# Kernel optimization log

Hardware: AMD Instinct MI355X
Metric: run time of the kernel (lower is better)

## Reference

```python
import jax, jax.numpy as jnp
import numpy as np

KW, KH = 8, 8   # kernel_size = (kw, kh) per torch module indexing
SW, SH = 4, 4   # stride_size = (sw, sh)


def setup_inputs() -> dict:
    key = jax.random.key(0)
    x = jax.random.normal(key, (4, 128, 128, 128), dtype=jnp.float32)  # [B, C, H, W]
    return {"x": x}


def _local_autocorr(x, kh=KH, kw=KW, sh=SH, sw=SW):
    B, C, H, W = x.shape
    nh = (H - kh) // sh + 1
    nw = (W - kw) // sw + 1
    # Background is x zero-padded by (kh//2, (kh+1)//2 - 1) vertically and
    # (kw//2, (kw+1)//2 - 1) horizontally -> background patches are (2kh-1, 2kw-1).
    xp = jnp.pad(x, ((0, 0), (0, 0),
                     (kh // 2, (kh + 1) // 2 - 1),
                     (kw // 2, (kw + 1) // 2 - 1)))

    # For each shift (dy, dx) in [0,kh)x[0,kw):
    #   ret[b,iy,ix,c,dy,dx] = sum_{u,v} x[b,c,top+u,left+v] * xp[b,c,top+dy+u,left+dx+v]
    # i.e. elementwise product with the shifted map, then sum-pool with window (kh,kw), stride (sh,sw).
    def step(carry, s):
        dy = s // kw
        dx = s % kw
        shifted = jax.lax.dynamic_slice(xp, (0, 0, dy, dx), (B, C, H, W))
        prod = x * shifted
        pooled = jax.lax.reduce_window(prod, 0.0, jax.lax.add,
                                       (1, 1, kh, kw), (1, 1, sh, sw), 'VALID')
        return carry, pooled  # [B, C, nh, nw]

    _, stacked = jax.lax.scan(step, None, jnp.arange(kh * kw))
    # stacked: [kh*kw, B, C, nh, nw] with shift index s = dy*kw + dx
    out = stacked.reshape(kh, kw, B, C, nh, nw)
    out = jnp.transpose(out, (2, 4, 5, 3, 0, 1))  # [B, nh, nw, C, kh, kw]
    return out


def reference(x):
    return _local_autocorr(x)
```

## Files before the change

### kernel.cpp

```cpp
#include <hip/hip_runtime.h>


#define Cn 128
#define Hn 128
#define Wn 128
#define NH 31
#define NW 31
#define CB 4
#define PXT 8
#define PYT 4
#define TROWS 27
#define RST 44
#define CSTF4 310
#define F4C (TROWS*11)

__global__ __launch_bounds__(256)
void lac_kernel(const float* __restrict__ x, float* __restrict__ out) {
    __shared__ float sm[CB * CSTF4 * 4];

    const int bid = blockIdx.x;
    const int lg = ((bid & 7) << 9) | (bid >> 3);
    const int tx = lg & 3;
    const int ty = (lg >> 2) & 7;
    const int ct = (lg >> 5) & 31;
    const int b  = lg >> 10;
    const int c0 = ct * CB;
    const int gy0 = ty * (PYT * 4) - 4;
    const int gx0 = tx * (PXT * 4) - 4;
    const int tid = threadIdx.x;

    const bool interior = (gy0 >= 0) & (gy0 + TROWS <= Hn) & (gx0 >= 0) & (gx0 + RST <= Wn);
    if (interior) {
        for (int i = tid; i < CB * F4C; i += 256) {
            const int c   = i / F4C;
            const int rem = i - c * F4C;
            const int r   = rem / 11;
            const int q   = rem - r * 11;
            const float* src = x + (((size_t)(b * Cn + c0 + c) * Hn + gy0 + r) * Wn + gx0 + q * 4);
            reinterpret_cast<float4*>(sm)[c * CSTF4 + r * 11 + q] =
                *reinterpret_cast<const float4*>(src);
        }
    } else {
        for (int i = tid; i < CB * F4C; i += 256) {
            const int c   = i / F4C;
            const int rem = i - c * F4C;
            const int r   = rem / 11;
            const int q   = rem - r * 11;
            const int y   = gy0 + r;
            const int xc  = gx0 + q * 4;
            const float* src = x + (((size_t)(b * Cn + c0 + c) * Hn + y) * Wn + xc);
            float4 v;
            if (y >= 0 && y < Hn && xc >= 0 && xc + 3 < Wn) {
                v = *reinterpret_cast<const float4*>(src);
            } else if (y >= 0 && y < Hn) {
                v.x = (xc + 0 >= 0 && xc + 0 < Wn) ? src[0] : 0.0f;
                v.y = (xc + 1 >= 0 && xc + 1 < Wn) ? src[1] : 0.0f;
                v.z = (xc + 2 >= 0 && xc + 2 < Wn) ? src[2] : 0.0f;
                v.w = (xc + 3 >= 0 && xc + 3 < Wn) ? src[3] : 0.0f;
            } else {
                v = make_float4(0.0f, 0.0f, 0.0f, 0.0f);
            }
            reinterpret_cast<float4*>(sm)[c * CSTF4 + r * 11 + q] = v;
        }
    }
    __syncthreads();

    const int cs   = tid & 3;
    const int px   = (tid >> 2) & 7;
    const int py   = (tid >> 5) & 3;
    const int half = tid >> 7;
    const float* rg = &sm[cs * (CSTF4 * 4) + (py * 4) * RST + px * 4];

    float acc[4][8];
#pragma unroll
    for (int i = 0; i < 4; ++i)
#pragma unroll
        for (int j = 0; j < 8; ++j) acc[i][j] = 0.0f;

    float ks[4][8];

#define LOAD_RW(R)                                                              \
    float rw[16];                                                               \
    {                                                                           \
        float4 q0 = *reinterpret_cast<const float4*>(&rg[(R) * RST + 0]);       \
        float4 q1 = *reinterpret_cast<const float4*>(&rg[(R) * RST + 4]);       \
        float4 q2 = *reinterpret_cast<const float4*>(&rg[(R) * RST + 8]);       \
        float4 q3 = *reinterpret_cast<const float4*>(&rg[(R) * RST + 12]);      \
        rw[0]=q0.x; rw[1]=q0.y; rw[2]=q0.z; rw[3]=q0.w;                         \
        rw[4]=q1.x; rw[5]=q1.y; rw[6]=q1.z; rw[7]=q1.w;                         \
        rw[8]=q2.x; rw[9]=q2.y; rw[10]=q2.z; rw[11]=q2.w;                       \
        rw[12]=q3.x; rw[13]=q3.y; rw[14]=q3.z; rw[15]=q3.w;                     \
    }

    if (half == 0) {
#pragma unroll
        for (int ii = 0; ii < 12; ++ii) {
            const int R = 11 - ii;
            LOAD_RW(R)
#pragma unroll
            for (int d = 0; d < 4; ++d) {
                if (R >= d && R <= 7 + d) {
#pragma unroll
                    for (int v = 0; v < 8; ++v) {
                        const float bv = ks[(R - d) & 3][v];
#pragma unroll
                        for (int dx = 0; dx < 8; ++dx)
                            acc[d][dx] = fmaf(bv, rw[dx + v], acc[d][dx]);
                    }
                }
            }
#pragma unroll
            for (int v = 0; v < 8; ++v) ks[R & 3][v] = rw[4 + v];
        }
    } else {
#pragma unroll
        for (int ii = 0; ii < 11; ++ii) {
            const int R = 4 + ii;
            LOAD_RW(R)
#pragma unroll
            for (int d = 0; d < 4; ++d) {
                if (R >= 4 + d && R <= 11 + d) {
#pragma unroll
                    for (int v = 0; v < 8; ++v) {
                        const float bv = (d == 0) ? rw[4 + v] : ks[(R - d) & 3][v];
#pragma unroll
                        for (int dx = 0; dx < 8; ++dx)
                            acc[d][dx] = fmaf(bv, rw[dx + v], acc[d][dx]);
                    }
                }
            }
#pragma unroll
            for (int v = 0; v < 8; ++v) ks[R & 3][v] = rw[4 + v];
        }
    }
#undef LOAD_RW

    const int iy = ty * PYT + py;
    const int ix = tx * PXT + px;
    if (iy < NH && ix < NW) {
        float* o = out + ((((size_t)b * NH + iy) * NW + ix) * Cn + (c0 + cs)) * 64
                       + half * 32;
#pragma unroll
        for (int d = 0; d < 4; ++d) {
            *reinterpret_cast<float4*>(o + d * 8 + 0) =
                make_float4(acc[d][0], acc[d][1], acc[d][2], acc[d][3]);
            *reinterpret_cast<float4*>(o + d * 8 + 4) =
                make_float4(acc[d][4], acc[d][5], acc[d][6], acc[d][7]);
        }
    }
}

extern "C" void kernel_launch(void* const* d_in, const int* in_sizes, int n_in,
                              void* d_out, int out_size, void* d_ws, size_t ws_size,
                              hipStream_t stream) {
    const float* x = (const float*)d_in[0];
    float* out = (float*)d_out;
    lac_kernel<<<dim3(4096), dim3(256), 0, stream>>>(x, out);
}
```

Baseline: 89.85 us.

## Load input rows directly from global memory, dropping shared-memory staging

Removes the cooperative shared-memory tile load and barrier, so each thread reads its 16-wide input rows straight from global memory with bounds handling per row. This eliminates LDS traffic, the sync, and the shared-memory footprint, which may raise occupancy. In exchange each input element is fetched several times by different threads and relies on L1/L2 caching, with less coalesced access since the four lanes sharing a pixel read different channel planes.

```diff
diff --git a/kernel.cpp b/kernel.cpp
--- a/kernel.cpp
+++ b/kernel.cpp
@@ -9,15 +9,10 @@
 #define CB 4
 #define PXT 8
 #define PYT 4
-#define TROWS 27
-#define RST 44
-#define CSTF4 310
-#define F4C (TROWS*11)
+#define RSPAN 43
 
 __global__ __launch_bounds__(256)
 void lac_kernel(const float* __restrict__ x, float* __restrict__ out) {
-    __shared__ float sm[CB * CSTF4 * 4];
-
     const int bid = blockIdx.x;
     const int lg = ((bid & 7) << 9) | (bid >> 3);
     const int tx = lg & 3;
@@ -29,47 +24,15 @@
     const int gx0 = tx * (PXT * 4) - 4;
     const int tid = threadIdx.x;
 
-    const bool interior = (gy0 >= 0) & (gy0 + TROWS <= Hn) & (gx0 >= 0) & (gx0 + RST <= Wn);
-    if (interior) {
-        for (int i = tid; i < CB * F4C; i += 256) {
-            const int c   = i / F4C;
-            const int rem = i - c * F4C;
-            const int r   = rem / 11;
-            const int q   = rem - r * 11;
-            const float* src = x + (((size_t)(b * Cn + c0 + c) * Hn + gy0 + r) * Wn + gx0 + q * 4);
-            reinterpret_cast<float4*>(sm)[c * CSTF4 + r * 11 + q] =
-                *reinterpret_cast<const float4*>(src);
-        }
-    } else {
-        for (int i = tid; i < CB * F4C; i += 256) {
-            const int c   = i / F4C;
-            const int rem = i - c * F4C;
-            const int r   = rem / 11;
-            const int q   = rem - r * 11;
-            const int y   = gy0 + r;
-            const int xc  = gx0 + q * 4;
-            const float* src = x + (((size_t)(b * Cn + c0 + c) * Hn + y) * Wn + xc);
-            float4 v;
-            if (y >= 0 && y < Hn && xc >= 0 && xc + 3 < Wn) {
-                v = *reinterpret_cast<const float4*>(src);
-            } else if (y >= 0 && y < Hn) {
-                v.x = (xc + 0 >= 0 && xc + 0 < Wn) ? src[0] : 0.0f;
-                v.y = (xc + 1 >= 0 && xc + 1 < Wn) ? src[1] : 0.0f;
-                v.z = (xc + 2 >= 0 && xc + 2 < Wn) ? src[2] : 0.0f;
-                v.w = (xc + 3 >= 0 && xc + 3 < Wn) ? src[3] : 0.0f;
-            } else {
-                v = make_float4(0.0f, 0.0f, 0.0f, 0.0f);
-            }
-            reinterpret_cast<float4*>(sm)[c * CSTF4 + r * 11 + q] = v;
-        }
-    }
-    __syncthreads();
-
     const int cs   = tid & 3;
     const int px   = (tid >> 2) & 7;
     const int py   = (tid >> 5) & 3;
     const int half = tid >> 7;
-    const float* rg = &sm[cs * (CSTF4 * 4) + (py * 4) * RST + px * 4];
+    const int c     = c0 + cs;
+    const int ybase = gy0 + py * 4;
+    const int xb    = gx0 + px * 4;
+    const float* xptr = x + (((ptrdiff_t)(b * Cn + c) * Hn + ybase) * Wn + xb);
+    const bool xsafe = (gx0 >= 0) && (gx0 + RSPAN <= Wn);
 
     float acc[4][8];
 #pragma unroll
@@ -79,24 +42,37 @@
 
     float ks[4][8];
 
-#define LOAD_RW(R)                                                              \
+#define LOAD_RW_G(R)                                                            \
     float rw[16];                                                               \
     {                                                                           \
-        float4 q0 = *reinterpret_cast<const float4*>(&rg[(R) * RST + 0]);       \
-        float4 q1 = *reinterpret_cast<const float4*>(&rg[(R) * RST + 4]);       \
-        float4 q2 = *reinterpret_cast<const float4*>(&rg[(R) * RST + 8]);       \
-        float4 q3 = *reinterpret_cast<const float4*>(&rg[(R) * RST + 12]);      \
-        rw[0]=q0.x; rw[1]=q0.y; rw[2]=q0.z; rw[3]=q0.w;                         \
-        rw[4]=q1.x; rw[5]=q1.y; rw[6]=q1.z; rw[7]=q1.w;                         \
-        rw[8]=q2.x; rw[9]=q2.y; rw[10]=q2.z; rw[11]=q2.w;                       \
-        rw[12]=q3.x; rw[13]=q3.y; rw[14]=q3.z; rw[15]=q3.w;                     \
+        const int yy = ybase + (R);                                             \
+        const float* rp = xptr + (ptrdiff_t)(R) * Wn;                           \
+        if ((unsigned)yy < (unsigned)Hn && xsafe) {                             \
+            float4 q0 = *reinterpret_cast<const float4*>(rp + 0);               \
+            float4 q1 = *reinterpret_cast<const float4*>(rp + 4);               \
+            float4 q2 = *reinterpret_cast<const float4*>(rp + 8);               \
+            float4 q3 = *reinterpret_cast<const float4*>(rp + 12);              \
+            rw[0]=q0.x; rw[1]=q0.y; rw[2]=q0.z; rw[3]=q0.w;                     \
+            rw[4]=q1.x; rw[5]=q1.y; rw[6]=q1.z; rw[7]=q1.w;                     \
+            rw[8]=q2.x; rw[9]=q2.y; rw[10]=q2.z; rw[11]=q2.w;                   \
+            rw[12]=q3.x; rw[13]=q3.y; rw[14]=q3.z; rw[15]=q3.w;                 \
+        } else if ((unsigned)yy < (unsigned)Hn) {                               \
+            _Pragma("unroll")                                                   \
+            for (int e = 0; e < 16; ++e) {                                      \
+                const int xe = xb + e;                                          \
+                rw[e] = ((unsigned)xe < (unsigned)Wn) ? rp[e] : 0.0f;           \
+            }                                                                   \
+        } else {                                                                \
+            _Pragma("unroll")                                                   \
+            for (int e = 0; e < 16; ++e) rw[e] = 0.0f;                          \
+        }                                                                       \
     }
 
     if (half == 0) {
 #pragma unroll
         for (int ii = 0; ii < 12; ++ii) {
             const int R = 11 - ii;
-            LOAD_RW(R)
+            LOAD_RW_G(R)
 #pragma unroll
             for (int d = 0; d < 4; ++d) {
                 if (R >= d && R <= 7 + d) {
@@ -116,7 +92,7 @@
 #pragma unroll
         for (int ii = 0; ii < 11; ++ii) {
             const int R = 4 + ii;
-            LOAD_RW(R)
+            LOAD_RW_G(R)
 #pragma unroll
             for (int d = 0; d < 4; ++d) {
                 if (R >= 4 + d && R <= 11 + d) {
@@ -133,12 +109,12 @@
             for (int v = 0; v < 8; ++v) ks[R & 3][v] = rw[4 + v];
         }
     }
-#undef LOAD_RW
+#undef LOAD_RW_G
 
     const int iy = ty * PYT + py;
     const int ix = tx * PXT + px;
     if (iy < NH && ix < NW) {
-        float* o = out + ((((size_t)b * NH + iy) * NW + ix) * Cn + (c0 + cs)) * 64
+        float* o = out + ((((size_t)b * NH + iy) * NW + ix) * Cn + c) * 64
                        + half * 32;
 #pragma unroll
         for (int d = 0; d < 4; ++d) {
```

Result: slower. 167.1 us (+86.0%).
